# Optimization experiments

Hardware: AMD Instinct MI355X
Metric: run time of the kernel (lower is better)

The kernel has to match this reference:

```python
import jax, jax.numpy as jnp
import numpy as np

B, R, CIN, J, O, ITERS = 512, 1152, 8, 10, 16, 3  # batch, routes, in_ch, capsules, out_ch, routing iters


def squash(s, axis):
    # v = (||s||^2 / (1 + ||s||^2)) * s / ||s||  (standard CapsNet squash)
    sq = jnp.sum(s * s, axis=axis, keepdims=True)
    return (sq / (1.0 + sq)) * s * jax.lax.rsqrt(sq + 1e-8)


def setup_inputs() -> dict:
    key = jax.random.key(0)
    k1, k2 = jax.random.split(key)
    x = jax.random.normal(k1, (B, R, CIN), dtype=jnp.float32)
    W = jax.random.normal(k2, (R, J, O, CIN), dtype=jnp.float32)  # param, batch-broadcast
    return {"x": x, "W": W}


def reference(x, W):
    # u_hat[b,r,j,:] = W[r,j] @ x[b,r]   (replaces torch stack/cat broadcasting)
    u_hat = jnp.einsum('rjoc,brc->brjo', W, x)  # [B,R,J,O]
    b_ij = jnp.zeros((x.shape[0], R, J), dtype=x.dtype)
    v = None
    for it in range(ITERS):
        c_ij = jax.nn.softmax(b_ij, axis=2)                 # softmax over capsules j
        s_j = jnp.einsum('brj,brjo->bjo', c_ij, u_hat)      # weighted sum over routes
        v = squash(s_j, axis=-1)                            # [B,J,O]
        if it < ITERS - 1:
            b_ij = b_ij + jnp.einsum('brjo,bjo->brj', u_hat, v)  # agreement
    # torch returns v_j.squeeze(1) with shape [B, J, O, 1]
    return v[..., None]
```

## Files before the change

kernel.cpp:

```cpp
#include <hip/hip_runtime.h>
#include <hip/hip_bf16.h>
#include <cstdint>
#include <cstddef>

#define NB 512
#define NR 1152
#define NC 8
#define NJ 10
#define NO 16
#define NJO 160

typedef unsigned int uint32;

__device__ __forceinline__ uint32 f2bf(float f) {
    uint32 x = __float_as_uint(f);
    return (x + 0x7fffu + ((x >> 16) & 1u)) >> 16;
}
__device__ __forceinline__ float bflo(uint32 w) { return __uint_as_float(w << 16); }
__device__ __forceinline__ float bfhi(uint32 w) { return __uint_as_float(w & 0xffff0000u); }

__global__ __launch_bounds__(256) void xpose_kernel(const float* __restrict__ x,
                                                    float* __restrict__ xT) {
    const int r0 = blockIdx.x * 16;
    const int b0 = blockIdx.y * 64;
    const int t  = threadIdx.x;
    __shared__ float tile[16][65][8];

    for (int i = t; i < 2048; i += 256) {
        int b = i >> 5, r = (i >> 1) & 15, h = i & 1;
        float4 v = *(const float4*)&x[(size_t)(b0 + b) * (NR * NC) + (size_t)(r0 + r) * NC + h * 4];
        *(float4*)&tile[r][b][h * 4] = v;
    }
    __syncthreads();
    for (int i = t; i < 2048; i += 256) {
        int r = i >> 7, b = (i >> 1) & 63, h = i & 1;
        float4 v = *(const float4*)&tile[r][b][h * 4];
        *(float4*)&xT[(size_t)(r0 + r) * (NB * NC) + (size_t)(b0 + b) * NC + h * 4] = v;
    }
}

__global__ __launch_bounds__(320) void uhat_kernel(const float* __restrict__ xT,
                                                   const float* __restrict__ W,
                                                   uint32* __restrict__ u) {
    const int r = blockIdx.x;
    const int t = threadIdx.x;

    __shared__ float Ws[NC][NJO];
    __shared__ float xs[NB][NC];

    for (int i = t; i < NJO * NC; i += 320) {
        Ws[i & 7][i >> 3] = W[(size_t)r * (NJO * NC) + i];
    }
    {
        const float4* xsrc = (const float4*)(xT + (size_t)r * (NB * NC));
        float4* xdst = (float4*)&xs[0][0];
        for (int i = t; i < (NB * NC) / 4; i += 320) xdst[i] = xsrc[i];
    }
    __syncthreads();

    const int jo2  = t % 80;
    const int half = t / 80;

    float w0[8], w1[8];
#pragma unroll
    for (int c = 0; c < 8; ++c) {
        w0[c] = Ws[c][2 * jo2];
        w1[c] = Ws[c][2 * jo2 + 1];
    }

    for (int b = half; b < NB; b += 4) {
        const float4* xp = (const float4*)xs[b];
        float4 xa = xp[0], xb = xp[1];
        float a0 = w0[0] * xa.x + w0[1] * xa.y + w0[2] * xa.z + w0[3] * xa.w
                 + w0[4] * xb.x + w0[5] * xb.y + w0[6] * xb.z + w0[7] * xb.w;
        float a1 = w1[0] * xa.x + w1[1] * xa.y + w1[2] * xa.z + w1[3] * xa.w
                 + w1[4] * xb.x + w1[5] * xb.y + w1[6] * xb.z + w1[7] * xb.w;
        uint32 p = f2bf(a0) | (f2bf(a1) << 16);
        u[(size_t)(b * NR + r) * 80 + jo2] = p;
    }
}

template <bool UNIFORM, bool FINAL>
__global__ __launch_bounds__(128, 1) void pass_kernel(const uint32* __restrict__ u,
                                                      const uint32* __restrict__ vsb,
                                                      float* __restrict__ vacc,
                                                      float* __restrict__ outp) {
    const int b    = blockIdx.x;
    const int t    = threadIdx.x;
    const int wv   = t >> 6;
    const int lane = t & 63;

    __shared__ float sl[NJO];
    for (int i = t; i < NJO; i += 128) sl[i] = 0.0f;
    __syncthreads();

    uint32 vs[80];
    if (!UNIFORM) {
        const uint4* vp = (const uint4*)(vsb + b * 80);
#pragma unroll
        for (int i = 0; i < 20; ++i) {
            uint4 q = vp[i];
            vs[4 * i + 0] = q.x; vs[4 * i + 1] = q.y;
            vs[4 * i + 2] = q.z; vs[4 * i + 3] = q.w;
        }
    }

    float acc[NJO];
#pragma unroll
    for (int i = 0; i < NJO; ++i) acc[i] = 0.0f;

#pragma unroll 1
    for (int c = 0; c < 9; ++c) {
        const int r = wv * 576 + c * 64 + lane;
        uint32 ur[80];
        const uint4* up = (const uint4*)(u + ((size_t)b * NR + r) * 80);
#pragma unroll
        for (int i = 0; i < 20; ++i) {
            uint4 q = up[i];
            ur[4 * i + 0] = q.x; ur[4 * i + 1] = q.y;
            ur[4 * i + 2] = q.z; ur[4 * i + 3] = q.w;
        }

        float cj[NJ];
        if (UNIFORM) {
#pragma unroll
            for (int j = 0; j < NJ; ++j) cj[j] = 0.1f;
        } else {
            float sum = 0.0f;
#pragma unroll
            for (int j = 0; j < NJ; ++j) {
                float bj = 0.0f;
#pragma unroll
                for (int q = 0; q < 8; ++q) {
                    uint32 uu = ur[8 * j + q], vv = vs[8 * j + q];
                    bj += bflo(uu) * bflo(vv) + bfhi(uu) * bfhi(vv);
                }
                float e = __expf(bj);
                cj[j] = e;
                sum += e;
            }
            float inv = 1.0f / sum;
#pragma unroll
            for (int j = 0; j < NJ; ++j) cj[j] *= inv;
        }

#pragma unroll
        for (int j = 0; j < NJ; ++j) {
#pragma unroll
            for (int q = 0; q < 8; ++q) {
                uint32 uu = ur[8 * j + q];
                acc[16 * j + 2 * q]     += cj[j] * bflo(uu);
                acc[16 * j + 2 * q + 1] += cj[j] * bfhi(uu);
            }
        }
    }

    float a[96];
    {
        const int bit = lane & 1;
#pragma unroll
        for (int i = 0; i < 96; ++i) {
            float lo = acc[i];
            float hi = (i < 64) ? acc[i + 96] : 0.0f;
            float send = bit ? lo : hi;
            float recv = __shfl_xor(send, 1);
            a[i] = (bit ? hi : lo) + recv;
        }
    }
#pragma unroll
    for (int st = 1; st < 6; ++st) {
        const int h = 96 >> st;
        const int bit = (lane >> st) & 1;
#pragma unroll
        for (int i = 0; i < 48; ++i) {
            if (i < h) {
                float send = bit ? a[i] : a[i + h];
                float recv = __shfl_xor(send, 1 << st);
                a[i] = (bit ? a[i + h] : a[i]) + recv;
            }
        }
    }

    const int base = 3 * (__brev((uint32)lane) >> 26);
#pragma unroll
    for (int i = 0; i < 3; ++i) {
        int jo = base + i;
        if (jo < NJO) atomicAdd(&sl[jo], a[i]);
    }
    __syncthreads();

    if (t < 80) {
        float2 sv = *(const float2*)&sl[2 * t];
        float sq = sv.x * sv.x + sv.y * sv.y;
#pragma unroll
        for (int off = 1; off < 8; off <<= 1) sq += __shfl_xor(sq, off, 8);
        float scale = (sq / (1.0f + sq)) * rsqrtf(sq + 1e-8f);
        float vx = sv.x * scale, vy = sv.y * scale;
        if (FINAL) {
            *(float2*)&outp[b * NJO + 2 * t] = make_float2(vx, vy);
        } else {
            float2 va = *(float2*)&vacc[b * NJO + 2 * t];
            va.x += vx; va.y += vy;
            *(float2*)&vacc[b * NJO + 2 * t] = va;
            ((uint32*)vsb)[b * 80 + t] = f2bf(va.x) | (f2bf(va.y) << 16);
        }
    }
}

extern "C" void kernel_launch(void* const* d_in, const int* in_sizes, int n_in,
                              void* d_out, int out_size, void* d_ws, size_t ws_size,
                              hipStream_t stream) {
    (void)in_sizes; (void)n_in; (void)out_size; (void)ws_size;

    const float* x = (const float*)d_in[0];
    const float* W = (const float*)d_in[1];
    float* out = (float*)d_out;

    char* ws = (char*)d_ws;
    const size_t XBYTES = (size_t)NR * NB * NC * 4;
    const size_t UBYTES = (size_t)NB * NR * NJO * 2;
    float*  xT   = (float*)ws;
    uint32* u    = (uint32*)(ws + XBYTES);
    float*  vacc = (float*)(ws + XBYTES + UBYTES);
    uint32* vsb  = (uint32*)(vacc + NB * NJO);

    hipMemsetAsync(vacc, 0, (size_t)NB * NJO * sizeof(float), stream);

    xpose_kernel<<<dim3(NR / 16, NB / 64), 256, 0, stream>>>(x, xT);
    uhat_kernel<<<NR, 320, 0, stream>>>(xT, W, u);

    pass_kernel<true, false><<<NB, 128, 0, stream>>>(u, vsb, vacc, nullptr);
    pass_kernel<false, false><<<NB, 128, 0, stream>>>(u, vsb, vacc, nullptr);
    pass_kernel<false, true><<<NB, 128, 0, stream>>>(u, vsb, nullptr, out);
}
```

Before: 240.4 us.

## Split each route across lane pairs and widen pass kernel to nine waves

Restructures the routing pass kernel from 128 threads per batch, each handling a whole route of 10 capsules, to 576 threads in which two lanes share a route and each takes 5 capsules. The softmax denominator is combined with a lane-pair shuffle. The routing vector is read from shared memory in fp32 instead of a bf16 register copy. This cuts per-thread register arrays roughly in half, which should raise occupancy and memory-level parallelism, and it drops the memset and the bf16 v buffer. In exchange the shuffle-reduction tree is restructured and atomics into shared memory grow with more waves per block.

```diff
diff --git a/kernel.cpp b/kernel.cpp
--- a/kernel.cpp
+++ b/kernel.cpp
@@ -1,5 +1,4 @@
 #include <hip/hip_runtime.h>
-#include <hip/hip_bf16.h>
 #include <cstdint>
 #include <cstddef>
 
@@ -80,112 +79,110 @@
     }
 }
 
-template <bool UNIFORM, bool FINAL>
-__global__ __launch_bounds__(128, 1) void pass_kernel(const uint32* __restrict__ u,
-                                                      const uint32* __restrict__ vsb,
+template <int MODE>
+__global__ __launch_bounds__(576, 2) void pass_kernel(const uint32* __restrict__ u,
                                                       float* __restrict__ vacc,
                                                       float* __restrict__ outp) {
-    const int b    = blockIdx.x;
-    const int t    = threadIdx.x;
-    const int wv   = t >> 6;
-    const int lane = t & 63;
-
+    const int b = blockIdx.x;
+    const int t = threadIdx.x;
+    const int w = t >> 6;
+    const int l = t & 63;
+    const int m = l >> 1;
+    const int h = l & 1;
+
+    __shared__ float vls[NJO];
     __shared__ float sl[NJO];
-    for (int i = t; i < NJO; i += 128) sl[i] = 0.0f;
-    __syncthreads();
-
-    uint32 vs[80];
-    if (!UNIFORM) {
-        const uint4* vp = (const uint4*)(vsb + b * 80);
-#pragma unroll
-        for (int i = 0; i < 20; ++i) {
-            uint4 q = vp[i];
-            vs[4 * i + 0] = q.x; vs[4 * i + 1] = q.y;
-            vs[4 * i + 2] = q.z; vs[4 * i + 3] = q.w;
-        }
-    }
-
-    float acc[NJO];
-#pragma unroll
-    for (int i = 0; i < NJO; ++i) acc[i] = 0.0f;
+    for (int i = t; i < NJO; i += 576) {
+        sl[i] = 0.0f;
+        if (MODE != 0) vls[i] = vacc[b * NJO + i];
+    }
+    __syncthreads();
+
+    float acc[80];
+#pragma unroll
+    for (int i = 0; i < 80; ++i) acc[i] = 0.0f;
+
+    const uint32* ubase = u + (size_t)b * (NR * 80);
 
 #pragma unroll 1
-    for (int c = 0; c < 9; ++c) {
-        const int r = wv * 576 + c * 64 + lane;
-        uint32 ur[80];
-        const uint4* up = (const uint4*)(u + ((size_t)b * NR + r) * 80);
-#pragma unroll
-        for (int i = 0; i < 20; ++i) {
+    for (int c4 = 0; c4 < 4; ++c4) {
+        const int c = 4 * w + c4;
+        const uint4* up = (const uint4*)(ubase + (size_t)c * 2560 + l * 40);
+        uint32 ur[40];
+#pragma unroll
+        for (int i = 0; i < 10; ++i) {
             uint4 q = up[i];
             ur[4 * i + 0] = q.x; ur[4 * i + 1] = q.y;
             ur[4 * i + 2] = q.z; ur[4 * i + 3] = q.w;
         }
 
-        float cj[NJ];
-        if (UNIFORM) {
-#pragma unroll
-            for (int j = 0; j < NJ; ++j) cj[j] = 0.1f;
+        float cj[5];
+        if (MODE == 0) {
+#pragma unroll
+            for (int j = 0; j < 5; ++j) cj[j] = 0.1f;
         } else {
-            float sum = 0.0f;
-#pragma unroll
-            for (int j = 0; j < NJ; ++j) {
+            float ej[5];
+            float ssum = 0.0f;
+#pragma unroll
+            for (int j = 0; j < 5; ++j) {
                 float bj = 0.0f;
 #pragma unroll
-                for (int q = 0; q < 8; ++q) {
-                    uint32 uu = ur[8 * j + q], vv = vs[8 * j + q];
-                    bj += bflo(uu) * bflo(vv) + bfhi(uu) * bfhi(vv);
+                for (int q8 = 0; q8 < 8; ++q8) {
+                    uint32 uu = ur[8 * j + q8];
+                    bj += bflo(uu) * vls[80 * h + 16 * j + 2 * q8]
+                        + bfhi(uu) * vls[80 * h + 16 * j + 2 * q8 + 1];
                 }
                 float e = __expf(bj);
-                cj[j] = e;
-                sum += e;
+                ej[j] = e;
+                ssum += e;
             }
-            float inv = 1.0f / sum;
-#pragma unroll
-            for (int j = 0; j < NJ; ++j) cj[j] *= inv;
-        }
-
-#pragma unroll
-        for (int j = 0; j < NJ; ++j) {
-#pragma unroll
-            for (int q = 0; q < 8; ++q) {
-                uint32 uu = ur[8 * j + q];
-                acc[16 * j + 2 * q]     += cj[j] * bflo(uu);
-                acc[16 * j + 2 * q + 1] += cj[j] * bfhi(uu);
+            ssum += __shfl_xor(ssum, 1);
+            float inv = 1.0f / ssum;
+#pragma unroll
+            for (int j = 0; j < 5; ++j) cj[j] = ej[j] * inv;
+        }
+
+#pragma unroll
+        for (int j = 0; j < 5; ++j) {
+#pragma unroll
+            for (int q8 = 0; q8 < 8; ++q8) {
+                uint32 uu = ur[8 * j + q8];
+                acc[16 * j + 2 * q8]     += cj[j] * bflo(uu);
+                acc[16 * j + 2 * q8 + 1] += cj[j] * bfhi(uu);
             }
         }
     }
 
-    float a[96];
+    float a[48];
     {
-        const int bit = lane & 1;
-#pragma unroll
-        for (int i = 0; i < 96; ++i) {
+        const int bit = (l >> 1) & 1;
+#pragma unroll
+        for (int i = 0; i < 48; ++i) {
             float lo = acc[i];
-            float hi = (i < 64) ? acc[i + 96] : 0.0f;
+            float hi = (i < 32) ? acc[i + 48] : 0.0f;
             float send = bit ? lo : hi;
-            float recv = __shfl_xor(send, 1);
+            float recv = __shfl_xor(send, 2);
             a[i] = (bit ? hi : lo) + recv;
         }
     }
 #pragma unroll
-    for (int st = 1; st < 6; ++st) {
-        const int h = 96 >> st;
-        const int bit = (lane >> st) & 1;
-#pragma unroll
-        for (int i = 0; i < 48; ++i) {
-            if (i < h) {
-                float send = bit ? a[i] : a[i + h];
-                float recv = __shfl_xor(send, 1 << st);
-                a[i] = (bit ? a[i + h] : a[i]) + recv;
+    for (int st = 1; st < 5; ++st) {
+        const int hw = 48 >> st;
+        const int bit = (l >> (st + 1)) & 1;
+#pragma unroll
+        for (int i = 0; i < 24; ++i) {
+            if (i < hw) {
+                float send = bit ? a[i] : a[i + hw];
+                float recv = __shfl_xor(send, 2 << st);
+                a[i] = (bit ? a[i + hw] : a[i]) + recv;
             }
         }
     }
-
-    const int base = 3 * (__brev((uint32)lane) >> 26);
+    const int base = 3 * (__brev((uint32)m) >> 27);
 #pragma unroll
     for (int i = 0; i < 3; ++i) {
-        int jo = base + i;
-        if (jo < NJO) atomicAdd(&sl[jo], a[i]);
+        int local = base + i;
+        if (local < 80) atomicAdd(&sl[80 * h + local], a[i]);
     }
     __syncthreads();
 
@@ -196,13 +193,13 @@
         for (int off = 1; off < 8; off <<= 1) sq += __shfl_xor(sq, off, 8);
         float scale = (sq / (1.0f + sq)) * rsqrtf(sq + 1e-8f);
         float vx = sv.x * scale, vy = sv.y * scale;
-        if (FINAL) {
+        if (MODE == 2) {
             *(float2*)&outp[b * NJO + 2 * t] = make_float2(vx, vy);
+        } else if (MODE == 1) {
+            float2 va = *(const float2*)&vacc[b * NJO + 2 * t];
+            *(float2*)&vacc[b * NJO + 2 * t] = make_float2(va.x + vx, va.y + vy);
         } else {
-            float2 va = *(float2*)&vacc[b * NJO + 2 * t];
-            va.x += vx; va.y += vy;
-            *(float2*)&vacc[b * NJO + 2 * t] = va;
-            ((uint32*)vsb)[b * 80 + t] = f2bf(va.x) | (f2bf(va.y) << 16);
+            *(float2*)&vacc[b * NJO + 2 * t] = make_float2(vx, vy);
         }
     }
 }
@@ -222,14 +219,11 @@
     float*  xT   = (float*)ws;
     uint32* u    = (uint32*)(ws + XBYTES);
     float*  vacc = (float*)(ws + XBYTES + UBYTES);
-    uint32* vsb  = (uint32*)(vacc + NB * NJO);
-
-    hipMemsetAsync(vacc, 0, (size_t)NB * NJO * sizeof(float), stream);
 
     xpose_kernel<<<dim3(NR / 16, NB / 64), 256, 0, stream>>>(x, xT);
     uhat_kernel<<<NR, 320, 0, stream>>>(xT, W, u);
 
-    pass_kernel<true, false><<<NB, 128, 0, stream>>>(u, vsb, vacc, nullptr);
-    pass_kernel<false, false><<<NB, 128, 0, stream>>>(u, vsb, vacc, nullptr);
-    pass_kernel<false, true><<<NB, 128, 0, stream>>>(u, vsb, nullptr, out);
-}
+    pass_kernel<0><<<NB, 576, 0, stream>>>(u, vacc, nullptr);
+    pass_kernel<1><<<NB, 576, 0, stream>>>(u, vacc, nullptr);
+    pass_kernel<2><<<NB, 576, 0, stream>>>(u, vacc, out);
+}
```

Result: slower. 502.6 us (+109.1%).
